# Performance work log

Hardware: AMD Instinct MI355X
Metric: run time of the kernel (lower is better)

Reference implementation:

```python
import jax, jax.numpy as jnp
import numpy as np

D_MODEL = 1024
NUM_HEADS = 16
D_K = D_MODEL // NUM_HEADS
B, S = 2, 2048
NEG = -1e9


def setup_inputs() -> dict:
    key = jax.random.key(0)
    ks = jax.random.split(key, 12)
    scale = 1.0 / np.sqrt(D_MODEL)
    inp = {
        'q': jax.random.normal(ks[0], (B, S, D_MODEL), jnp.float32),
        'k': jax.random.normal(ks[1], (B, S, D_MODEL), jnp.float32),
        'v': jax.random.normal(ks[2], (B, S, D_MODEL), jnp.float32),
        'mask': jax.random.randint(ks[3], (1, 1, S, S), 0, 2, jnp.int32),
        'wq_w': jax.random.normal(ks[4], (D_MODEL, D_MODEL), jnp.float32) * scale,
        'wq_b': jnp.zeros((D_MODEL,), jnp.float32),
        'wk_w': jax.random.normal(ks[5], (D_MODEL, D_MODEL), jnp.float32) * scale,
        'wk_b': jnp.zeros((D_MODEL,), jnp.float32),
        'wv_w': jax.random.normal(ks[6], (D_MODEL, D_MODEL), jnp.float32) * scale,
        'wv_b': jnp.zeros((D_MODEL,), jnp.float32),
        'wo_w': jax.random.normal(ks[7], (D_MODEL, D_MODEL), jnp.float32) * scale,
        'wo_b': jnp.zeros((D_MODEL,), jnp.float32),
    }
    return inp


def _split_heads(x):
    # [B,S,D] -> [B,H,S,d_k]
    b, s, _ = x.shape
    return x.reshape(b, s, NUM_HEADS, D_K).transpose(0, 2, 1, 3)


def reference(q, k, v, mask, wq_w, wq_b, wk_w, wk_b, wv_w, wv_b, wo_w, wo_b):
    # torch Linear: y = x @ W.T + b
    qh = _split_heads(q @ wq_w.T + wq_b)
    kh = _split_heads(k @ wk_w.T + wk_b)
    vh = _split_heads(v @ wv_w.T + wv_b)
    scores = jnp.einsum('bhqd,bhkd->bhqk', qh, kh) / jnp.sqrt(jnp.float32(D_K))
    scores = jnp.where(mask == 0, jnp.float32(NEG), scores)
    attn = jax.nn.softmax(scores, axis=-1)  # dropout p=0 (eval): no-op
    x = jnp.einsum('bhqk,bhkd->bhqd', attn, vh)
    x = x.transpose(0, 2, 1, 3).reshape(q.shape[0], q.shape[1], D_MODEL)
    return x @ wo_w.T + wo_b
```

## Files before the change

kernel.cpp:

```cpp
#include <hip/hip_runtime.h>
#include <hip/hip_bf16.h>
#include <stdint.h>

#define S_LEN  2048
#define DMODEL 1024
#define NHEADS 16
#define DKH    64
#define KDIM   1024

typedef __bf16 bf16x8 __attribute__((ext_vector_type(8)));
typedef short  short4v __attribute__((ext_vector_type(4)));
typedef float  floatx4 __attribute__((ext_vector_type(4)));
typedef unsigned short ushort8v __attribute__((ext_vector_type(8)));

__device__ inline void gll16(const __bf16* g, const __bf16* l) {
    __builtin_amdgcn_global_load_lds(
        (const __attribute__((address_space(1))) void*)g,
        (__attribute__((address_space(3))) void*)l, 16, 0, 0);
}

__global__ __launch_bounds__(256) void convert_all_kernel(
    const float* __restrict__ q, const float* __restrict__ k, const float* __restrict__ v,
    const float* __restrict__ wq, const float* __restrict__ wk, const float* __restrict__ wv,
    const float* __restrict__ wo, __bf16* __restrict__ out) {
    const size_t i8 = ((size_t)blockIdx.x * 256 + threadIdx.x) * 8;
    const float* src;
    if (i8 < 4194304u)        src = q  + i8;
    else if (i8 < 8388608u)   src = k  + (i8 - 4194304u);
    else if (i8 < 12582912u)  src = v  + (i8 - 8388608u);
    else if (i8 < 13631488u)  src = wq + (i8 - 12582912u);
    else if (i8 < 14680064u)  src = wk + (i8 - 13631488u);
    else if (i8 < 15728640u)  src = wv + (i8 - 14680064u);
    else                      src = wo + (i8 - 15728640u);
    floatx4 a = *(const floatx4*)src;
    floatx4 b = *(const floatx4*)(src + 4);
    bf16x8 r;
#pragma unroll
    for (int i = 0; i < 4; ++i) { r[i] = (__bf16)a[i]; r[i + 4] = (__bf16)b[i]; }
    *(bf16x8*)(out + i8) = r;
}

__global__ __launch_bounds__(256) void maskpack_kernel(const int* __restrict__ M,
                                                       uint64_t* __restrict__ P) {
    const size_t i = (size_t)blockIdx.x * 256 + threadIdx.x;
    uint64_t bits = __ballot(M[i] != 0);
    if ((threadIdx.x & 63) == 0) P[i >> 6] = bits;
}

template <int MODE, typename TC>
__global__ __launch_bounds__(256) void gemm_nt(const __bf16* __restrict__ A,
                                               const __bf16* __restrict__ Bm,
                                               const float* __restrict__ bias,
                                               TC* __restrict__ C) {
    __shared__ __align__(16) __bf16 As[2 * 128 * 32];
    __shared__ __align__(16) __bf16 Bs[2 * 128 * 32];

    const int lane = threadIdx.x & 63;
    const int wave = threadIdx.x >> 6;
    const int quad = lane >> 4;
    const int l15  = lane & 15;
    const int m_t = blockIdx.y * 128, n_t = blockIdx.x * 128;
    const int m0w = (wave >> 1) * 64, n0w = (wave & 1) * 64;

    const int sp = wave >> 1;
    const int sr = (wave & 1) * 64;
    const int lrow = lane >> 2;
    const int lcol = (lane & 3) * 8;

    floatx4 acc[4][4];
#pragma unroll
    for (int i = 0; i < 4; ++i)
#pragma unroll
        for (int j = 0; j < 4; ++j)
            acc[i][j] = (floatx4){0.f, 0.f, 0.f, 0.f};

    for (int kk = 0; kk < KDIM; kk += 64) {
#pragma unroll
        for (int c = 0; c < 4; ++c) {
            const int row = sr + c * 16 + lrow;
            gll16(A + (size_t)(m_t + row) * KDIM + kk + sp * 32 + lcol,
                  As + (sp * 128 + sr + c * 16) * 32);
            gll16(Bm + (size_t)(n_t + row) * KDIM + kk + sp * 32 + lcol,
                  Bs + (sp * 128 + sr + c * 16) * 32);
        }
        __syncthreads();
#pragma unroll
        for (int p = 0; p < 2; ++p) {
            bf16x8 af[4], bfr[4];
#pragma unroll
            for (int i = 0; i < 4; ++i)
                af[i] = *(const bf16x8*)(As + ((p * 128 + m0w + i * 16 + l15) * 32 + quad * 8));
#pragma unroll
            for (int j = 0; j < 4; ++j)
                bfr[j] = *(const bf16x8*)(Bs + ((p * 128 + n0w + j * 16 + l15) * 32 + quad * 8));
#pragma unroll
            for (int i = 0; i < 4; ++i)
#pragma unroll
                for (int j = 0; j < 4; ++j)
                    acc[i][j] = __builtin_amdgcn_mfma_f32_16x16x32_bf16(af[i], bfr[j], acc[i][j], 0, 0, 0);
        }
        __syncthreads();
    }

#pragma unroll
    for (int j = 0; j < 4; ++j) {
        const int n = n_t + n0w + j * 16 + l15;
        float bn = (MODE == 1) ? 0.f : bias[n];
#pragma unroll
        for (int i = 0; i < 4; ++i) {
#pragma unroll
            for (int r = 0; r < 4; ++r) {
                const int m = m_t + m0w + i * 16 + quad * 4 + r;
                float bv = (MODE == 1) ? bias[m] : bn;
                float v = acc[i][j][r] + bv;
                size_t off;
                if (MODE == 0) {
                    off = ((size_t)((m >> 11) * 16 + (n >> 6)) * 2048 + (m & 2047)) * 64 + (n & 63);
                } else if (MODE == 1) {
                    off = ((size_t)((n >> 11) * 16 + (m >> 6)) * 64 + (m & 63)) * 2048 + (n & 2047);
                } else {
                    off = (size_t)m * 1024 + n;
                }
                C[off] = (TC)v;
            }
        }
    }
}

__global__ __launch_bounds__(256) void attn_kernel(const __bf16* __restrict__ Qh,
                                                   const __bf16* __restrict__ Kh,
                                                   const __bf16* __restrict__ Vt,
                                                   const uint64_t* __restrict__ PM,
                                                   __bf16* __restrict__ X) {
    __shared__ __align__(16) __bf16 Ks[2][4096];
    __shared__ __align__(16) __bf16 Vs[2][4096];
    __shared__ __align__(16) unsigned short xls[4][16][80];

    const int lane = threadIdx.x & 63;
    const int wave = threadIdx.x >> 6;
    const int quad = lane >> 4;
    const int l15  = lane & 15;

    const int bid  = blockIdx.x;
    const int xcd  = bid & 7;
    const int slot = bid >> 3;
    const int grp  = xcd * 4 + (slot >> 4);
    const int qt   = slot & 15;
    const int b = grp >> 4, h = grp & 15;
    const int q0 = qt * 128 + wave * 32;

    const __bf16* Qb = Qh + (size_t)(b * NHEADS + h) * S_LEN * DKH;
    const __bf16* Kb = Kh + (size_t)(b * NHEADS + h) * S_LEN * DKH;
    const __bf16* Vb = Vt + (size_t)(b * NHEADS + h) * DKH * S_LEN;
    const uint64_t* pr0 = PM + (size_t)(q0 + l15) * (S_LEN / 64);
    const uint64_t* pr1 = PM + (size_t)(q0 + 16 + l15) * (S_LEN / 64);

    const float cs = 0.18033688011112042f;
    const float MB = 4.0f;

    size_t offK[2], offV[2];
    const __bf16* ldsK[2];
    const __bf16* ldsV[2];
#pragma unroll
    for (int i = 0; i < 2; ++i) {
        const int s = wave * 128 + i * 64 + lane;
        const int r = s >> 3, cp = s & 7, c = cp ^ (r & 7);
        offK[i] = (size_t)r * DKH + c * 8;
        offV[i] = (size_t)r * S_LEN + c * 8;
    }
#pragma unroll
    for (int i = 0; i < 2; ++i) {
        ldsK[i] = nullptr; ldsV[i] = nullptr;
    }

    bf16x8 qf[2][2];
#pragma unroll
    for (int s = 0; s < 2; ++s)
#pragma unroll
        for (int c = 0; c < 2; ++c)
            qf[s][c] = *(const bf16x8*)(Qb + (size_t)(q0 + s * 16 + l15) * DKH + c * 32 + quad * 8);

    floatx4 o[2][4];
#pragma unroll
    for (int s = 0; s < 2; ++s)
#pragma unroll
        for (int f = 0; f < 4; ++f) o[s][f] = (floatx4){0.f, 0.f, 0.f, 0.f};
    float lsum[2] = {0.f, 0.f};

    auto stage = [&](int p, int key0) {
#pragma unroll
        for (int i = 0; i < 2; ++i) {
            gll16(Kb + (size_t)key0 * DKH + offK[i], &Ks[p][(wave * 128 + i * 64) * 8]);
            gll16(Vb + key0 + offV[i],               &Vs[p][(wave * 128 + i * 64) * 8]);
        }
    };

    stage(0, 0);
    for (int kt = 0; kt < 32; ++kt) {
        const int p = kt & 1;
        __syncthreads();
        if (kt < 31) stage(p ^ 1, (kt + 1) * 64);

        const uint64_t mw0 = pr0[kt];
        const uint64_t mw1 = pr1[kt];

        bf16x8 kf[4][2];
#pragma unroll
        for (int t = 0; t < 4; ++t) {
            const int rr = t * 16 + l15;
#pragma unroll
            for (int hh = 0; hh < 2; ++hh) {
                const int cp = (hh * 4 + quad) ^ (l15 & 7);
                kf[t][hh] = *(const bf16x8*)&Ks[p][rr * 64 + cp * 8];
            }
        }

        floatx4 st[2][4];
#pragma unroll
        for (int s = 0; s < 2; ++s)
#pragma unroll
            for (int t = 0; t < 4; ++t) {
                floatx4 z = (floatx4){0.f, 0.f, 0.f, 0.f};
                z = __builtin_amdgcn_mfma_f32_16x16x32_bf16(kf[t][0], qf[s][0], z, 0, 0, 0);
                z = __builtin_amdgcn_mfma_f32_16x16x32_bf16(kf[t][1], qf[s][1], z, 0, 0, 0);
                st[s][t] = z;
            }

        short4v pt[2][4];
#pragma unroll
        for (int s = 0; s < 2; ++s) {
            const uint64_t mw = s ? mw1 : mw0;
#pragma unroll
            for (int t = 0; t < 4; ++t) {
                const int sh = t * 16 + quad * 4;
                short4v pp;
#pragma unroll
                for (int r = 0; r < 4; ++r) {
                    float e = exp2f(fmaf(st[s][t][r], cs, -MB));
                    e = ((mw >> (sh + r)) & 1u) ? e : 0.f;
                    lsum[s] += e;
                    __bf16 pb = (__bf16)e;
                    pp[r] = __builtin_bit_cast(short, pb);
                }
                pt[s][t] = pp;
            }
        }

#pragma unroll
        for (int t = 0; t < 4; ++t) {
#pragma unroll
            for (int f = 0; f < 4; ++f) {
                const int r = f * 16 + l15;
                const int cp = (t * 2 + (quad >> 1)) ^ (l15 & 7);
                short4v vfr = *(const short4v*)&Vs[p][r * 64 + cp * 8 + (quad & 1) * 4];
#pragma unroll
                for (int s = 0; s < 2; ++s)
                    o[s][f] = __builtin_amdgcn_mfma_f32_16x16x16bf16_1k(vfr, pt[s][t], o[s][f], 0, 0, 0);
            }
        }
    }

    float inv[2];
#pragma unroll
    for (int s = 0; s < 2; ++s) {
        float t = lsum[s];
        t += __shfl_xor(t, 16);
        t += __shfl_xor(t, 32);
        inv[s] = (t > 0.f) ? (1.f / t) : 0.f;
    }

#pragma unroll
    for (int s = 0; s < 2; ++s) {
#pragma unroll
        for (int f = 0; f < 4; ++f)
#pragma unroll
            for (int r = 0; r < 4; ++r) {
                __bf16 bv = (__bf16)(o[s][f][r] * inv[s]);
                xls[wave][l15][f * 16 + quad * 4 + r] = __builtin_bit_cast(unsigned short, bv);
            }
#pragma unroll
        for (int it = 0; it < 2; ++it) {
            const int ql = it * 8 + (lane >> 3);
            const int dseg = (lane & 7) * 8;
            ushort8v vv = *(const ushort8v*)&xls[wave][ql][dseg];
            unsigned short* dst = (unsigned short*)X +
                (size_t)(b * S_LEN + q0 + s * 16 + ql) * DMODEL + h * DKH + dseg;
            *(ushort8v*)dst = vv;
        }
    }
}

extern "C" void kernel_launch(void* const* d_in, const int* in_sizes, int n_in,
                              void* d_out, int out_size, void* d_ws, size_t ws_size,
                              hipStream_t stream) {
    const float* q   = (const float*)d_in[0];
    const float* k   = (const float*)d_in[1];
    const float* v   = (const float*)d_in[2];
    const int*   msk = (const int*)d_in[3];
    const float* wq  = (const float*)d_in[4];
    const float* wqb = (const float*)d_in[5];
    const float* wk  = (const float*)d_in[6];
    const float* wkb = (const float*)d_in[7];
    const float* wv  = (const float*)d_in[8];
    const float* wvb = (const float*)d_in[9];
    const float* wo  = (const float*)d_in[10];
    const float* wob = (const float*)d_in[11];

    char* ws = (char*)d_ws;
    __bf16*   qh   = (__bf16*)(ws);
    __bf16*   kh   = (__bf16*)(ws + 8388608);
    __bf16*   vt   = (__bf16*)(ws + 16777216);
    uint64_t* pm   = (uint64_t*)(ws + 25165824);
    __bf16*   cb   = (__bf16*)(ws + 25690112);
    __bf16*   qb   = cb;
    __bf16*   kb   = cb + 4194304;
    __bf16*   vb   = cb + 8388608;
    __bf16*   wqbf = cb + 12582912;
    __bf16*   wkbf = cb + 13631488;
    __bf16*   wvbf = cb + 14680064;
    __bf16*   wobf = cb + 15728640;
    __bf16*   xa   = qb;

    convert_all_kernel<<<8192, 256, 0, stream>>>(q, k, v, wq, wk, wv, wo, cb);
    maskpack_kernel<<<16384, 256, 0, stream>>>(msk, pm);
    gemm_nt<0, __bf16><<<dim3(8, 32), 256, 0, stream>>>(qb, wqbf, wqb, qh);
    gemm_nt<0, __bf16><<<dim3(8, 32), 256, 0, stream>>>(kb, wkbf, wkb, kh);
    gemm_nt<1, __bf16><<<dim3(32, 8), 256, 0, stream>>>(wvbf, vb, wvb, vt);
    attn_kernel<<<512, 256, 0, stream>>>(qh, kh, vt, pm, xa);
    gemm_nt<2, float><<<dim3(8, 32), 256, 0, stream>>>(xa, wobf, wob, (float*)d_out);
}
```

Before: 315.0 us.

## Fuse QKV GEMMs, swizzle LDS, use K=32 MFMA in attention, retile output GEMM

The three QKV projection GEMMs become one 768-block launch, cutting launch overhead and improving occupancy. Both GEMMs get an XOR swizzle on LDS columns to reduce bank conflicts. The output projection uses 128x64 tiles, giving 512 blocks instead of 256 to fill more CUs. The attention PV product moves from 16x16x16 to 16x16x32 MFMA, with the K rows permuted so the probability layout matches, and the output staging buffer now reuses the K shared-memory region. The permutation is subtle and risks correctness errors.

```diff
diff --git a/kernel.cpp b/kernel.cpp
--- a/kernel.cpp
+++ b/kernel.cpp
@@ -9,7 +9,6 @@
 #define KDIM   1024
 
 typedef __bf16 bf16x8 __attribute__((ext_vector_type(8)));
-typedef short  short4v __attribute__((ext_vector_type(4)));
 typedef float  floatx4 __attribute__((ext_vector_type(4)));
 typedef unsigned short ushort8v __attribute__((ext_vector_type(8)));
 
@@ -47,11 +46,11 @@
     if ((threadIdx.x & 63) == 0) P[i >> 6] = bits;
 }
 
-template <int MODE, typename TC>
-__global__ __launch_bounds__(256) void gemm_nt(const __bf16* __restrict__ A,
-                                               const __bf16* __restrict__ Bm,
-                                               const float* __restrict__ bias,
-                                               TC* __restrict__ C) {
+__global__ __launch_bounds__(256) void qkv_gemm(
+    const __bf16* __restrict__ qb, const __bf16* __restrict__ kb, const __bf16* __restrict__ vb,
+    const __bf16* __restrict__ wqw, const __bf16* __restrict__ wkw, const __bf16* __restrict__ wvw,
+    const float* __restrict__ biasq, const float* __restrict__ biask, const float* __restrict__ biasv,
+    __bf16* __restrict__ qh, __bf16* __restrict__ kh, __bf16* __restrict__ vt) {
     __shared__ __align__(16) __bf16 As[2 * 128 * 32];
     __shared__ __align__(16) __bf16 Bs[2 * 128 * 32];
 
@@ -59,13 +58,23 @@
     const int wave = threadIdx.x >> 6;
     const int quad = lane >> 4;
     const int l15  = lane & 15;
-    const int m_t = blockIdx.y * 128, n_t = blockIdx.x * 128;
+
+    const int bid = blockIdx.x;
+    const int job = bid >> 8;
+    const int tt  = bid & 255;
+    const __bf16* A; const __bf16* Bm; const float* bias; __bf16* C;
+    int bx, by, MODE;
+    if (job == 0)      { A = qb;  Bm = wqw; bias = biasq; C = qh; bx = tt & 7;  by = tt >> 3; MODE = 0; }
+    else if (job == 1) { A = kb;  Bm = wkw; bias = biask; C = kh; bx = tt & 7;  by = tt >> 3; MODE = 0; }
+    else               { A = wvw; Bm = vb;  bias = biasv; C = vt; bx = tt & 31; by = tt >> 5; MODE = 1; }
+
+    const int m_t = by * 128, n_t = bx * 128;
     const int m0w = (wave >> 1) * 64, n0w = (wave & 1) * 64;
 
     const int sp = wave >> 1;
     const int sr = (wave & 1) * 64;
     const int lrow = lane >> 2;
-    const int lcol = (lane & 3) * 8;
+    const int scol = ((lane & 3) ^ (lrow & 3)) * 8;
 
     floatx4 acc[4][4];
 #pragma unroll
@@ -78,21 +87,22 @@
 #pragma unroll
         for (int c = 0; c < 4; ++c) {
             const int row = sr + c * 16 + lrow;
-            gll16(A + (size_t)(m_t + row) * KDIM + kk + sp * 32 + lcol,
+            gll16(A + (size_t)(m_t + row) * KDIM + kk + sp * 32 + scol,
                   As + (sp * 128 + sr + c * 16) * 32);
-            gll16(Bm + (size_t)(n_t + row) * KDIM + kk + sp * 32 + lcol,
+            gll16(Bm + (size_t)(n_t + row) * KDIM + kk + sp * 32 + scol,
                   Bs + (sp * 128 + sr + c * 16) * 32);
         }
         __syncthreads();
+        const int cq = (quad ^ (l15 & 3)) * 8;
 #pragma unroll
         for (int p = 0; p < 2; ++p) {
             bf16x8 af[4], bfr[4];
 #pragma unroll
             for (int i = 0; i < 4; ++i)
-                af[i] = *(const bf16x8*)(As + ((p * 128 + m0w + i * 16 + l15) * 32 + quad * 8));
+                af[i] = *(const bf16x8*)(As + (p * 128 + m0w + i * 16 + l15) * 32 + cq);
 #pragma unroll
             for (int j = 0; j < 4; ++j)
-                bfr[j] = *(const bf16x8*)(Bs + ((p * 128 + n0w + j * 16 + l15) * 32 + quad * 8));
+                bfr[j] = *(const bf16x8*)(Bs + (p * 128 + n0w + j * 16 + l15) * 32 + cq);
 #pragma unroll
             for (int i = 0; i < 4; ++i)
 #pragma unroll
@@ -116,14 +126,84 @@
                 size_t off;
                 if (MODE == 0) {
                     off = ((size_t)((m >> 11) * 16 + (n >> 6)) * 2048 + (m & 2047)) * 64 + (n & 63);
-                } else if (MODE == 1) {
+                } else {
                     off = ((size_t)((n >> 11) * 16 + (m >> 6)) * 64 + (m & 63)) * 2048 + (n & 2047);
-                } else {
-                    off = (size_t)m * 1024 + n;
                 }
-                C[off] = (TC)v;
-            }
-        }
+                C[off] = (__bf16)v;
+            }
+        }
+    }
+}
+
+__global__ __launch_bounds__(256) void gemm_out(const __bf16* __restrict__ A,
+                                                const __bf16* __restrict__ Bm,
+                                                const float* __restrict__ bias,
+                                                float* __restrict__ C) {
+    __shared__ __align__(16) __bf16 As[2 * 128 * 32];
+    __shared__ __align__(16) __bf16 Bs[2 * 64 * 32];
+
+    const int lane = threadIdx.x & 63;
+    const int wave = threadIdx.x >> 6;
+    const int quad = lane >> 4;
+    const int l15  = lane & 15;
+    const int m_t = blockIdx.y * 128, n_t = blockIdx.x * 64;
+    const int m0w = (wave >> 1) * 64, n0w = (wave & 1) * 32;
+
+    const int lrow = lane >> 2;
+    const int scol = ((lane & 3) ^ (lrow & 3)) * 8;
+
+    floatx4 acc[4][2];
+#pragma unroll
+    for (int i = 0; i < 4; ++i)
+#pragma unroll
+        for (int j = 0; j < 2; ++j)
+            acc[i][j] = (floatx4){0.f, 0.f, 0.f, 0.f};
+
+    for (int kk = 0; kk < KDIM; kk += 64) {
+#pragma unroll
+        for (int u = 0; u < 6; ++u) {
+            const int pi = wave * 6 + u;
+            if (pi < 16) {
+                const int panel = pi >> 3, rb = pi & 7;
+                gll16(A + (size_t)(m_t + rb * 16 + lrow) * KDIM + kk + panel * 32 + scol,
+                      As + (panel * 128 + rb * 16) * 32);
+            } else {
+                const int qi = pi - 16, panel = qi >> 2, rb = qi & 3;
+                gll16(Bm + (size_t)(n_t + rb * 16 + lrow) * KDIM + kk + panel * 32 + scol,
+                      Bs + (panel * 64 + rb * 16) * 32);
+            }
+        }
+        __syncthreads();
+        const int cq = (quad ^ (l15 & 3)) * 8;
+#pragma unroll
+        for (int p = 0; p < 2; ++p) {
+            bf16x8 af[4], bfr[2];
+#pragma unroll
+            for (int i = 0; i < 4; ++i)
+                af[i] = *(const bf16x8*)(As + (p * 128 + m0w + i * 16 + l15) * 32 + cq);
+#pragma unroll
+            for (int j = 0; j < 2; ++j)
+                bfr[j] = *(const bf16x8*)(Bs + (p * 64 + n0w + j * 16 + l15) * 32 + cq);
+#pragma unroll
+            for (int i = 0; i < 4; ++i)
+#pragma unroll
+                for (int j = 0; j < 2; ++j)
+                    acc[i][j] = __builtin_amdgcn_mfma_f32_16x16x32_bf16(af[i], bfr[j], acc[i][j], 0, 0, 0);
+        }
+        __syncthreads();
+    }
+
+#pragma unroll
+    for (int j = 0; j < 2; ++j) {
+        const int n = n_t + n0w + j * 16 + l15;
+        const float bn = bias[n];
+#pragma unroll
+        for (int i = 0; i < 4; ++i)
+#pragma unroll
+            for (int r = 0; r < 4; ++r) {
+                const int m = m_t + m0w + i * 16 + quad * 4 + r;
+                C[(size_t)m * 1024 + n] = acc[i][j][r] + bn;
+            }
     }
 }
 
@@ -134,12 +214,12 @@
                                                    __bf16* __restrict__ X) {
     __shared__ __align__(16) __bf16 Ks[2][4096];
     __shared__ __align__(16) __bf16 Vs[2][4096];
-    __shared__ __align__(16) unsigned short xls[4][16][80];
 
     const int lane = threadIdx.x & 63;
     const int wave = threadIdx.x >> 6;
     const int quad = lane >> 4;
     const int l15  = lane & 15;
+    const int l7   = l15 & 7;
 
     const int bid  = blockIdx.x;
     const int xcd  = bid & 7;
@@ -159,18 +239,13 @@
     const float MB = 4.0f;
 
     size_t offK[2], offV[2];
-    const __bf16* ldsK[2];
-    const __bf16* ldsV[2];
 #pragma unroll
     for (int i = 0; i < 2; ++i) {
         const int s = wave * 128 + i * 64 + lane;
         const int r = s >> 3, cp = s & 7, c = cp ^ (r & 7);
-        offK[i] = (size_t)r * DKH + c * 8;
+        const int kr = (r >> 5) * 32 + ((r >> 4) & 1) * 4 + ((r >> 2) & 3) * 8 + (r & 3);
+        offK[i] = (size_t)kr * DKH + c * 8;
         offV[i] = (size_t)r * S_LEN + c * 8;
-    }
-#pragma unroll
-    for (int i = 0; i < 2; ++i) {
-        ldsK[i] = nullptr; ldsV[i] = nullptr;
     }
 
     bf16x8 qf[2][2];
@@ -206,14 +281,12 @@
 
         bf16x8 kf[4][2];
 #pragma unroll
-        for (int t = 0; t < 4; ++t) {
-            const int rr = t * 16 + l15;
+        for (int t = 0; t < 4; ++t)
 #pragma unroll
             for (int hh = 0; hh < 2; ++hh) {
-                const int cp = (hh * 4 + quad) ^ (l15 & 7);
-                kf[t][hh] = *(const bf16x8*)&Ks[p][rr * 64 + cp * 8];
-            }
-        }
+                const int cp = ((hh * 4 + quad) ^ l7) * 8;
+                kf[t][hh] = *(const bf16x8*)&Ks[p][(t * 16 + l15) * 64 + cp];
+            }
 
         floatx4 st[2][4];
 #pragma unroll
@@ -226,36 +299,37 @@
                 st[s][t] = z;
             }
 
-        short4v pt[2][4];
+        bf16x8 pw[2][2];
 #pragma unroll
         for (int s = 0; s < 2; ++s) {
             const uint64_t mw = s ? mw1 : mw0;
 #pragma unroll
-            for (int t = 0; t < 4; ++t) {
-                const int sh = t * 16 + quad * 4;
-                short4v pp;
-#pragma unroll
-                for (int r = 0; r < 4; ++r) {
-                    float e = exp2f(fmaf(st[s][t][r], cs, -MB));
-                    e = ((mw >> (sh + r)) & 1u) ? e : 0.f;
-                    lsum[s] += e;
-                    __bf16 pb = (__bf16)e;
-                    pp[r] = __builtin_bit_cast(short, pb);
+            for (int w = 0; w < 2; ++w) {
+                bf16x8 pb;
+#pragma unroll
+                for (int half = 0; half < 2; ++half) {
+                    const int t = w * 2 + half;
+                    const int sh = w * 32 + half * 4 + quad * 8;
+#pragma unroll
+                    for (int r = 0; r < 4; ++r) {
+                        float e = exp2f(fmaf(st[s][t][r], cs, -MB));
+                        e = ((mw >> (sh + r)) & 1u) ? e : 0.f;
+                        lsum[s] += e;
+                        pb[half * 4 + r] = (__bf16)e;
+                    }
                 }
-                pt[s][t] = pp;
-            }
-        }
-
-#pragma unroll
-        for (int t = 0; t < 4; ++t) {
+                pw[s][w] = pb;
+            }
+        }
+
+#pragma unroll
+        for (int w = 0; w < 2; ++w) {
+            const int cp = ((w * 4 + quad) ^ l7) * 8;
 #pragma unroll
             for (int f = 0; f < 4; ++f) {
-                const int r = f * 16 + l15;
-                const int cp = (t * 2 + (quad >> 1)) ^ (l15 & 7);
-                short4v vfr = *(const short4v*)&Vs[p][r * 64 + cp * 8 + (quad & 1) * 4];
-#pragma unroll
-                for (int s = 0; s < 2; ++s)
-                    o[s][f] = __builtin_amdgcn_mfma_f32_16x16x16bf16_1k(vfr, pt[s][t], o[s][f], 0, 0, 0);
+                bf16x8 vf = *(const bf16x8*)&Vs[p][(f * 16 + l15) * 64 + cp];
+                o[0][f] = __builtin_amdgcn_mfma_f32_16x16x32_bf16(vf, pw[0][w], o[0][f], 0, 0, 0);
+                o[1][f] = __builtin_amdgcn_mfma_f32_16x16x32_bf16(vf, pw[1][w], o[1][f], 0, 0, 0);
             }
         }
     }
@@ -269,6 +343,8 @@
         inv[s] = (t > 0.f) ? (1.f / t) : 0.f;
     }
 
+    __syncthreads();
+    unsigned short* xw = (unsigned short*)&Ks[0][0] + wave * (16 * 80);
 #pragma unroll
     for (int s = 0; s < 2; ++s) {
 #pragma unroll
@@ -276,13 +352,13 @@
 #pragma unroll
             for (int r = 0; r < 4; ++r) {
                 __bf16 bv = (__bf16)(o[s][f][r] * inv[s]);
-                xls[wave][l15][f * 16 + quad * 4 + r] = __builtin_bit_cast(unsigned short, bv);
+                xw[l15 * 80 + f * 16 + quad * 4 + r] = __builtin_bit_cast(unsigned short, bv);
             }
 #pragma unroll
         for (int it = 0; it < 2; ++it) {
             const int ql = it * 8 + (lane >> 3);
             const int dseg = (lane & 7) * 8;
-            ushort8v vv = *(const ushort8v*)&xls[wave][ql][dseg];
+            ushort8v vv = *(const ushort8v*)&xw[ql * 80 + dseg];
             unsigned short* dst = (unsigned short*)X +
                 (size_t)(b * S_LEN + q0 + s * 16 + ql) * DMODEL + h * DKH + dseg;
             *(ushort8v*)dst = vv;
@@ -323,9 +399,7 @@
 
     convert_all_kernel<<<8192, 256, 0, stream>>>(q, k, v, wq, wk, wv, wo, cb);
     maskpack_kernel<<<16384, 256, 0, stream>>>(msk, pm);
-    gemm_nt<0, __bf16><<<dim3(8, 32), 256, 0, stream>>>(qb, wqbf, wqb, qh);
-    gemm_nt<0, __bf16><<<dim3(8, 32), 256, 0, stream>>>(kb, wkbf, wkb, kh);
-    gemm_nt<1, __bf16><<<dim3(32, 8), 256, 0, stream>>>(wvbf, vb, wvb, vt);
+    qkv_gemm<<<768, 256, 0, stream>>>(qb, kb, vb, wqbf, wkbf, wvbf, wqb, wkb, wvb, qh, kh, vt);
     attn_kernel<<<512, 256, 0, stream>>>(qh, kh, vt, pm, xa);
-    gemm_nt<2, float><<<dim3(8, 32), 256, 0, stream>>>(xa, wobf, wob, (float*)d_out);
-}
+    gemm_out<<<dim3(16, 32), 256, 0, stream>>>(xa, wobf, wob, (float*)d_out);
+}
```

After: 296.4 us. 5.9% less time.
